# Optimization experiments

Hardware: AMD Instinct MI355X
Metric: run time of the kernel (lower is better)

## Reference

```python
import jax, jax.numpy as jnp
import numpy as np

TOP_K = 2


def setup_inputs() -> dict:
    key = jax.random.key(0)
    k1, k2, k3, k4, k5 = jax.random.split(key, 5)
    B, S, H, I, E = 2, 2048, 1024, 1408, 8
    scale = 0.02
    return {
        "hidden_states": jax.random.normal(k1, (B, S, H), dtype=jnp.float32),
        "router_w": jax.random.normal(k2, (E, H), dtype=jnp.float32) * scale,
        "w_gate": jax.random.normal(k3, (E, I, H), dtype=jnp.float32) * scale,
        "w_up": jax.random.normal(k4, (E, I, H), dtype=jnp.float32) * scale,
        "w_down": jax.random.normal(k5, (E, H, I), dtype=jnp.float32) * scale,
    }


def reference(hidden_states, router_w, w_gate, w_up, w_down):
    B, S, H = hidden_states.shape
    E = router_w.shape[0]
    x = hidden_states.reshape(-1, H)  # [T, H]

    # Router: softmax over experts, take top-k, renormalize.
    probs = jax.nn.softmax(x @ router_w.T, axis=-1)          # [T, E]
    topk_w, topk_idx = jax.lax.top_k(probs, TOP_K)            # [T, k]
    topk_w = topk_w / (jnp.sum(topk_w, axis=-1, keepdims=True) + 1e-20)

    # Dense combine weights: zero for non-selected experts -> identical math
    # to the masked gather/scatter loop in the original module.
    combine = jnp.sum(
        topk_w[..., None] * jax.nn.one_hot(topk_idx, E, dtype=topk_w.dtype),
        axis=1,
    )  # [T, E]

    out = jnp.zeros_like(x)
    for e in range(E):  # small fixed expert count; unrolled under jit
        g = x @ w_gate[e].T                                   # [T, I]
        u = x @ w_up[e].T                                     # [T, I]
        ye = (jax.nn.silu(g) * u) @ w_down[e].T               # [T, H]
        out = out + combine[:, e:e + 1] * ye
    return out.reshape(B, S, H)
```

## Files before the change

kernel.cpp:

```cpp
#include <hip/hip_runtime.h>
#include <hip/hip_bf16.h>

#define T_TOK 4096
#define H_DIM 1024
#define I_DIM 1408
#define E_NUM 8
#define P_CAP 8192
#define GRID_Y 71

typedef __bf16 bf16;
typedef __bf16 bf16x4 __attribute__((ext_vector_type(4)));
typedef __bf16 bf16x8 __attribute__((ext_vector_type(8)));
typedef float  f32x4  __attribute__((ext_vector_type(4)));

__device__ __forceinline__ void load_lds16(const void* g, void* l) {
  __builtin_amdgcn_global_load_lds((const __attribute__((address_space(1))) void*)g,
                                   (__attribute__((address_space(3))) void*)l, 16, 0, 0);
}

__global__ __launch_bounds__(256) void cast_all(const float* __restrict__ x,
                                                const float* __restrict__ wg,
                                                const float* __restrict__ wu,
                                                const float* __restrict__ wd,
                                                bf16* __restrict__ xb, bf16* __restrict__ wgb,
                                                bf16* __restrict__ wub, bf16* __restrict__ wdb) {
  int b = blockIdx.x;
  const float* s; bf16* d; int base;
  if (b < 4096)       { s = x;  d = xb;  base = b; }
  else if (b < 15360) { s = wg; d = wgb; base = b - 4096; }
  else if (b < 26624) { s = wu; d = wub; base = b - 15360; }
  else                { s = wd; d = wdb; base = b - 26624; }
  size_t i = ((size_t)base * 256 + threadIdx.x) * 4;
  float4 v = *(const float4*)(s + i);
  bf16x4 o;
  o.x = (bf16)v.x; o.y = (bf16)v.y; o.z = (bf16)v.z; o.w = (bf16)v.w;
  *(bf16x4*)(d + i) = o;
}

__global__ __launch_bounds__(256) void router_kernel(const float* __restrict__ x,
                                                     const float* __restrict__ rw,
                                                     int* __restrict__ tidx,
                                                     float* __restrict__ tw) {
  int t = blockIdx.x * 4 + (threadIdx.x >> 6);
  int lane = threadIdx.x & 63;
  const float* xr = x + (size_t)t * H_DIM;
  float acc[E_NUM];
#pragma unroll
  for (int e = 0; e < E_NUM; ++e) acc[e] = 0.f;
  for (int c = lane; c < H_DIM; c += 64) {
    float xv = xr[c];
#pragma unroll
    for (int e = 0; e < E_NUM; ++e) acc[e] += xv * rw[e * H_DIM + c];
  }
#pragma unroll
  for (int e = 0; e < E_NUM; ++e)
    for (int s = 32; s > 0; s >>= 1) acc[e] += __shfl_down(acc[e], s, 64);
  if (lane == 0) {
    int a = 0;
#pragma unroll
    for (int e = 1; e < E_NUM; ++e) if (acc[e] > acc[a]) a = e;
    int b = (a == 0) ? 1 : 0;
#pragma unroll
    for (int e = 0; e < E_NUM; ++e) if (e != a && acc[e] > acc[b]) b = e;
    float pb = expf(acc[b] - acc[a]);
    float inv = 1.f / (1.f + pb);
    tidx[t * 2] = a; tidx[t * 2 + 1] = b;
    tw[t * 2] = inv; tw[t * 2 + 1] = pb * inv;
  }
}

__global__ __launch_bounds__(256) void bucket_kernel(const int* __restrict__ tidx,
                                                     const float* __restrict__ tw,
                                                     int* __restrict__ pair_tok,
                                                     float* __restrict__ pair_w,
                                                     int* __restrict__ counts,
                                                     int* __restrict__ offsets,
                                                     int* __restrict__ blk2e,
                                                     int* __restrict__ blk2m) {
  __shared__ int sc[E_NUM], so[E_NUM], scur[E_NUM];
  int tid = threadIdx.x;
  if (tid < E_NUM) sc[tid] = 0;
  __syncthreads();
  for (int p = tid; p < T_TOK * 2; p += 256) atomicAdd(&sc[tidx[p]], 1);
  __syncthreads();
  if (tid == 0) {
    int run = 0, nb = 0;
    for (int e = 0; e < E_NUM; ++e) {
      so[e] = run; run += sc[e];
      for (int m = 0; m * 128 < sc[e]; ++m) { blk2e[nb] = e; blk2m[nb] = m; ++nb; }
    }
    for (; nb < GRID_Y; ++nb) { blk2e[nb] = -1; blk2m[nb] = 0; }
  }
  __syncthreads();
  if (tid < E_NUM) scur[tid] = so[tid];
  __syncthreads();
  for (int t = tid; t < T_TOK; t += 256) {
#pragma unroll
    for (int k = 0; k < 2; ++k) {
      int e = tidx[t * 2 + k];
      int pos = atomicAdd(&scur[e], 1);
      pair_tok[pos] = t;
      pair_w[pos] = tw[t * 2 + k];
    }
  }
  if (tid < E_NUM) { counts[tid] = sc[tid]; offsets[tid] = so[tid]; }
}

__global__ __launch_bounds__(256, 2)
void gemm1_kernel(const bf16* __restrict__ xb, const bf16* __restrict__ wgb,
                  const bf16* __restrict__ wub, const int* __restrict__ pair_tok,
                  const int* __restrict__ counts, const int* __restrict__ offsets,
                  const int* __restrict__ blk2e, const int* __restrict__ blk2m,
                  bf16* __restrict__ mid) {
  const int e = blk2e[blockIdx.y];
  if (e < 0) return;
  const int cnt = counts[e];
  const int m0 = blk2m[blockIdx.y] << 7;
  const int off = offsets[e];
  const int n0 = blockIdx.x << 7;

  __shared__ bf16 As[128 * 64];
  __shared__ bf16 Bgs[128 * 64];
  __shared__ bf16 Bus[128 * 64];

  const int tid = threadIdx.x;
  const int wave = tid >> 6;
  const int lane = tid & 63;
  const int wm = (wave >> 1) << 6;
  const int wn = (wave & 1) << 6;

  const bf16* wg_e = wgb + (size_t)e * (I_DIM * H_DIM);
  const bf16* wu_e = wub + (size_t)e * (I_DIM * H_DIM);

  int arow[4], acs[4], atok[4];
#pragma unroll
  for (int j = 0; j < 4; ++j) {
    int seg = ((wave << 2) + j) * 64 + lane;
    int row = seg >> 3;
    arow[j] = row;
    acs[j]  = ((seg & 7) ^ (row & 7)) << 3;
    int gr = m0 + row;
    int cr = gr < cnt ? gr : cnt - 1;
    atok[j] = pair_tok[off + cr];
  }

  f32x4 accg[4][4], accu[4][4];
#pragma unroll
  for (int i = 0; i < 4; ++i)
#pragma unroll
    for (int j = 0; j < 4; ++j) {
      accg[i][j] = (f32x4){0.f, 0.f, 0.f, 0.f};
      accu[i][j] = (f32x4){0.f, 0.f, 0.f, 0.f};
    }

  const int lr = lane & 15;
  const int sw = lr & 7;
  const int qd = lane >> 4;

  for (int k0 = 0; k0 < H_DIM; k0 += 64) {
#pragma unroll
    for (int j = 0; j < 4; ++j) {
      int base = ((wave << 2) + j) << 9;
      load_lds16(xb + (size_t)atok[j] * H_DIM + k0 + acs[j], As + base);
      load_lds16(wg_e + (size_t)(n0 + arow[j]) * H_DIM + k0 + acs[j], Bgs + base);
      load_lds16(wu_e + (size_t)(n0 + arow[j]) * H_DIM + k0 + acs[j], Bus + base);
    }
    __syncthreads();
#pragma unroll
    for (int ks = 0; ks < 2; ++ks) {
      const int kc = (((ks << 2) + qd) ^ sw) << 3;
      bf16x8 a[4], bg[4], bu[4];
#pragma unroll
      for (int i = 0; i < 4; ++i)
        a[i] = *(const bf16x8*)(As + (wm + (i << 4) + lr) * 64 + kc);
#pragma unroll
      for (int j = 0; j < 4; ++j) {
        bg[j] = *(const bf16x8*)(Bgs + (wn + (j << 4) + lr) * 64 + kc);
        bu[j] = *(const bf16x8*)(Bus + (wn + (j << 4) + lr) * 64 + kc);
      }
#pragma unroll
      for (int i = 0; i < 4; ++i)
#pragma unroll
        for (int j = 0; j < 4; ++j) {
          accg[i][j] = __builtin_amdgcn_mfma_f32_16x16x32_bf16(a[i], bg[j], accg[i][j], 0, 0, 0);
          accu[i][j] = __builtin_amdgcn_mfma_f32_16x16x32_bf16(a[i], bu[j], accu[i][j], 0, 0, 0);
        }
    }
    __syncthreads();
  }

#pragma unroll
  for (int i = 0; i < 4; ++i) {
#pragma unroll
    for (int r = 0; r < 4; ++r) {
      int row = wm + (i << 4) + (qd << 2) + r;
      int gr = m0 + row;
      if (gr < cnt) {
        bf16* mrow = mid + (size_t)(off + gr) * I_DIM + n0 + wn;
#pragma unroll
        for (int j = 0; j < 4; ++j) {
          float g = accg[i][j][r], u = accu[i][j][r];
          float s = g / (1.f + __expf(-g));
          mrow[(j << 4) + lr] = (bf16)(s * u);
        }
      }
    }
  }
}

__global__ __launch_bounds__(256, 2)
void gemm2_kernel(const bf16* __restrict__ mid, const bf16* __restrict__ wdb,
                  const int* __restrict__ pair_tok, const float* __restrict__ pair_w,
                  const int* __restrict__ counts, const int* __restrict__ offsets,
                  const int* __restrict__ blk2e, const int* __restrict__ blk2m,
                  float* __restrict__ out) {
  const int e = blk2e[blockIdx.y];
  if (e < 0) return;
  const int cnt = counts[e];
  const int m0 = blk2m[blockIdx.y] << 7;
  const int off = offsets[e];
  const int n0 = blockIdx.x << 7;

  __shared__ bf16 As[128 * 64];
  __shared__ bf16 Bs[128 * 64];

  const int tid = threadIdx.x;
  const int wave = tid >> 6;
  const int lane = tid & 63;
  const int wm = (wave >> 1) << 6;
  const int wn = (wave & 1) << 6;

  const bf16* wd_e = wdb + (size_t)e * (H_DIM * I_DIM);

  int arow[4], acs[4];
  size_t apos[4];
#pragma unroll
  for (int j = 0; j < 4; ++j) {
    int seg = ((wave << 2) + j) * 64 + lane;
    int row = seg >> 3;
    arow[j] = row;
    acs[j]  = ((seg & 7) ^ (row & 7)) << 3;
    int gr = m0 + row;
    int cr = gr < cnt ? gr : cnt - 1;
    apos[j] = (size_t)(off + cr) * I_DIM + acs[j];
  }

  f32x4 acc[4][4];
#pragma unroll
  for (int i = 0; i < 4; ++i)
#pragma unroll
    for (int j = 0; j < 4; ++j) acc[i][j] = (f32x4){0.f, 0.f, 0.f, 0.f};

  const int lr = lane & 15;
  const int sw = lr & 7;
  const int qd = lane >> 4;

  for (int k0 = 0; k0 < I_DIM; k0 += 64) {
#pragma unroll
    for (int j = 0; j < 4; ++j) {
      int base = ((wave << 2) + j) << 9;
      load_lds16(mid + apos[j] + k0, As + base);
      load_lds16(wd_e + (size_t)(n0 + arow[j]) * I_DIM + k0 + acs[j], Bs + base);
    }
    __syncthreads();
#pragma unroll
    for (int ks = 0; ks < 2; ++ks) {
      const int kc = (((ks << 2) + qd) ^ sw) << 3;
      bf16x8 a[4], b[4];
#pragma unroll
      for (int i = 0; i < 4; ++i)
        a[i] = *(const bf16x8*)(As + (wm + (i << 4) + lr) * 64 + kc);
#pragma unroll
      for (int j = 0; j < 4; ++j)
        b[j] = *(const bf16x8*)(Bs + (wn + (j << 4) + lr) * 64 + kc);
#pragma unroll
      for (int i = 0; i < 4; ++i)
#pragma unroll
        for (int j = 0; j < 4; ++j)
          acc[i][j] = __builtin_amdgcn_mfma_f32_16x16x32_bf16(a[i], b[j], acc[i][j], 0, 0, 0);
    }
    __syncthreads();
  }

#pragma unroll
  for (int i = 0; i < 4; ++i) {
#pragma unroll
    for (int r = 0; r < 4; ++r) {
      int row = wm + (i << 4) + (qd << 2) + r;
      int gr = m0 + row;
      if (gr < cnt) {
        int t = pair_tok[off + gr];
        float w = pair_w[off + gr];
        float* orow = out + (size_t)t * H_DIM + n0 + wn;
#pragma unroll
        for (int j = 0; j < 4; ++j)
          atomicAdd(orow + (j << 4) + lr, w * acc[i][j][r]);
      }
    }
  }
}

extern "C" void kernel_launch(void* const* d_in, const int* in_sizes, int n_in,
                              void* d_out, int out_size, void* d_ws, size_t ws_size,
                              hipStream_t stream) {
  const float* x  = (const float*)d_in[0];
  const float* rw = (const float*)d_in[1];
  const float* wg = (const float*)d_in[2];
  const float* wu = (const float*)d_in[3];
  const float* wd = (const float*)d_in[4];
  float* out = (float*)d_out;

  char* ws = (char*)d_ws;
  bf16*  xb      = (bf16*)(ws);
  bf16*  wgb     = (bf16*)(ws + 8388608);
  bf16*  wub     = (bf16*)(ws + 31457280);
  bf16*  wdb     = (bf16*)(ws + 54525952);
  bf16*  mid     = (bf16*)(ws + 77594624);
  int*   tidx    = (int*)(ws + 100663296);
  float* tw      = (float*)(ws + 100696064);
  int*   ptok    = (int*)(ws + 100728832);
  float* pw      = (float*)(ws + 100761600);
  int*   counts  = (int*)(ws + 100794368);
  int*   offsets = (int*)(ws + 100794400);
  int*   blk2e   = (int*)(ws + 100794432);
  int*   blk2m   = (int*)(ws + 100794752);

  hipMemsetAsync(d_out, 0, (size_t)T_TOK * H_DIM * sizeof(float), stream);
  cast_all<<<37888, 256, 0, stream>>>(x, wg, wu, wd, xb, wgb, wub, wdb);
  router_kernel<<<1024, 256, 0, stream>>>(x, rw, tidx, tw);
  bucket_kernel<<<1, 256, 0, stream>>>(tidx, tw, ptok, pw, counts, offsets, blk2e, blk2m);
  gemm1_kernel<<<dim3(11, GRID_Y), 256, 0, stream>>>(xb, wgb, wub, ptok, counts, offsets, blk2e, blk2m, mid);
  gemm2_kernel<<<dim3(8, GRID_Y), 256, 0, stream>>>(mid, wdb, ptok, pw, counts, offsets, blk2e, blk2m, out);
}
```

Before: 345.8 us.

## Replace atomic scatter with per-pair output buffer and gather combine kernel

gemm2 now writes each expert-pair result row to a dense fp32 buffer (reusing the wgb region, which is dead by then), and a new combine kernel gathers the two rows per token and applies the routing weights. This removes the output memset and the fp32 atomicAdd scatter. Block scheduling changes to a flattened, XCD-interleaved schedule table so blocks sharing an expert's weights land on the same chiplet. Bucketing uses wave ballots, and the router uses float4 loads. The cost is an extra 32MB write and read of intermediates plus one more kernel launch.

```diff
diff --git a/kernel.cpp b/kernel.cpp
--- a/kernel.cpp
+++ b/kernel.cpp
@@ -6,7 +6,8 @@
 #define I_DIM 1408
 #define E_NUM 8
 #define P_CAP 8192
-#define GRID_Y 71
+#define G1_GRID 1136
+#define G2_GRID 568
 
 typedef __bf16 bf16;
 typedef __bf16 bf16x4 __attribute__((ext_vector_type(4)));
@@ -43,14 +44,18 @@
                                                      float* __restrict__ tw) {
   int t = blockIdx.x * 4 + (threadIdx.x >> 6);
   int lane = threadIdx.x & 63;
-  const float* xr = x + (size_t)t * H_DIM;
+  const float4* xr  = (const float4*)(x + (size_t)t * H_DIM);
+  const float4* rw4 = (const float4*)rw;
   float acc[E_NUM];
 #pragma unroll
   for (int e = 0; e < E_NUM; ++e) acc[e] = 0.f;
-  for (int c = lane; c < H_DIM; c += 64) {
-    float xv = xr[c];
-#pragma unroll
-    for (int e = 0; e < E_NUM; ++e) acc[e] += xv * rw[e * H_DIM + c];
+  for (int c = lane; c < H_DIM / 4; c += 64) {
+    float4 xv = xr[c];
+#pragma unroll
+    for (int e = 0; e < E_NUM; ++e) {
+      float4 rv = rw4[e * (H_DIM / 4) + c];
+      acc[e] += xv.x * rv.x + xv.y * rv.y + xv.z * rv.z + xv.w * rv.w;
+    }
   }
 #pragma unroll
   for (int e = 0; e < E_NUM; ++e)
@@ -70,54 +75,90 @@
 }
 
 __global__ __launch_bounds__(256) void bucket_kernel(const int* __restrict__ tidx,
-                                                     const float* __restrict__ tw,
                                                      int* __restrict__ pair_tok,
-                                                     float* __restrict__ pair_w,
+                                                     int* __restrict__ inv,
                                                      int* __restrict__ counts,
                                                      int* __restrict__ offsets,
-                                                     int* __restrict__ blk2e,
-                                                     int* __restrict__ blk2m) {
+                                                     int* __restrict__ sched1,
+                                                     int* __restrict__ sched2) {
   __shared__ int sc[E_NUM], so[E_NUM], scur[E_NUM];
-  int tid = threadIdx.x;
+  int tid = threadIdx.x, lane = tid & 63, wv = tid >> 6;
   if (tid < E_NUM) sc[tid] = 0;
+  for (int i = tid; i < G1_GRID; i += 256) sched1[i] = -1;
+  for (int i = tid; i < G2_GRID; i += 256) sched2[i] = -1;
   __syncthreads();
-  for (int p = tid; p < T_TOK * 2; p += 256) atomicAdd(&sc[tidx[p]], 1);
+  int local[E_NUM];
+#pragma unroll
+  for (int e = 0; e < E_NUM; ++e) local[e] = 0;
+  for (int base = wv * 64; base < P_CAP; base += 256) {
+    int e = tidx[base + lane];
+#pragma unroll
+    for (int x = 0; x < E_NUM; ++x)
+      local[x] += __popcll(__ballot(e == x));
+  }
+  if (lane == 0) {
+#pragma unroll
+    for (int x = 0; x < E_NUM; ++x) atomicAdd(&sc[x], local[x]);
+  }
   __syncthreads();
   if (tid == 0) {
-    int run = 0, nb = 0;
-    for (int e = 0; e < E_NUM; ++e) {
-      so[e] = run; run += sc[e];
-      for (int m = 0; m * 128 < sc[e]; ++m) { blk2e[nb] = e; blk2m[nb] = m; ++nb; }
-    }
-    for (; nb < GRID_Y; ++nb) { blk2e[nb] = -1; blk2m[nb] = 0; }
+    int run = 0;
+    for (int e = 0; e < E_NUM; ++e) { so[e] = run; run += sc[e]; }
+    int q1[8] = {0,0,0,0,0,0,0,0};
+    for (int c = 0; c < 88; ++c) {
+      int e = c / 11, n0 = c % 11, k = c % 8;
+      for (int m = 0; m * 128 < sc[e]; ++m) {
+        sched1[q1[k] * 8 + k] = (e << 16) | (m << 8) | n0;
+        ++q1[k];
+      }
+    }
+    int q2[8] = {0,0,0,0,0,0,0,0};
+    for (int c = 0; c < 64; ++c) {
+      int e = c >> 3, n0 = c & 7, k = n0;
+      for (int m = 0; m * 128 < sc[e]; ++m) {
+        sched2[q2[k] * 8 + k] = (e << 16) | (m << 8) | n0;
+        ++q2[k];
+      }
+    }
   }
   __syncthreads();
-  if (tid < E_NUM) scur[tid] = so[tid];
+  if (tid < E_NUM) { scur[tid] = so[tid]; counts[tid] = sc[tid]; offsets[tid] = so[tid]; }
   __syncthreads();
-  for (int t = tid; t < T_TOK; t += 256) {
-#pragma unroll
-    for (int k = 0; k < 2; ++k) {
-      int e = tidx[t * 2 + k];
-      int pos = atomicAdd(&scur[e], 1);
-      pair_tok[pos] = t;
-      pair_w[pos] = tw[t * 2 + k];
-    }
-  }
-  if (tid < E_NUM) { counts[tid] = sc[tid]; offsets[tid] = so[tid]; }
+  for (int base = wv * 64; base < P_CAP; base += 256) {
+    int p = base + lane;
+    int e = tidx[p];
+#pragma unroll
+    for (int x = 0; x < E_NUM; ++x) {
+      bool mine = (e == x);
+      unsigned long long m = __ballot(mine);
+      if (m == 0) continue;
+      int leader = __ffsll((long long)m) - 1;
+      int n = __popcll(m);
+      int bpos = 0;
+      if (lane == leader) bpos = atomicAdd(&scur[x], n);
+      bpos = __shfl(bpos, leader, 64);
+      if (mine) {
+        int rank = __popcll(m & ((1ull << lane) - 1ull));
+        int pos = bpos + rank;
+        pair_tok[pos] = p >> 1;
+        inv[p] = pos;
+      }
+    }
+  }
 }
 
 __global__ __launch_bounds__(256, 2)
 void gemm1_kernel(const bf16* __restrict__ xb, const bf16* __restrict__ wgb,
                   const bf16* __restrict__ wub, const int* __restrict__ pair_tok,
                   const int* __restrict__ counts, const int* __restrict__ offsets,
-                  const int* __restrict__ blk2e, const int* __restrict__ blk2m,
-                  bf16* __restrict__ mid) {
-  const int e = blk2e[blockIdx.y];
-  if (e < 0) return;
+                  const int* __restrict__ sched1, bf16* __restrict__ mid) {
+  const int sv = sched1[blockIdx.x];
+  if (sv < 0) return;
+  const int e  = sv >> 16;
+  const int m0 = ((sv >> 8) & 0xff) << 7;
+  const int n0 = (sv & 0xff) << 7;
   const int cnt = counts[e];
-  const int m0 = blk2m[blockIdx.y] << 7;
   const int off = offsets[e];
-  const int n0 = blockIdx.x << 7;
 
   __shared__ bf16 As[128 * 64];
   __shared__ bf16 Bgs[128 * 64];
@@ -210,16 +251,15 @@
 
 __global__ __launch_bounds__(256, 2)
 void gemm2_kernel(const bf16* __restrict__ mid, const bf16* __restrict__ wdb,
-                  const int* __restrict__ pair_tok, const float* __restrict__ pair_w,
                   const int* __restrict__ counts, const int* __restrict__ offsets,
-                  const int* __restrict__ blk2e, const int* __restrict__ blk2m,
-                  float* __restrict__ out) {
-  const int e = blk2e[blockIdx.y];
-  if (e < 0) return;
+                  const int* __restrict__ sched2, float* __restrict__ ybuf) {
+  const int sv = sched2[blockIdx.x];
+  if (sv < 0) return;
+  const int e  = sv >> 16;
+  const int m0 = ((sv >> 8) & 0xff) << 7;
+  const int n0 = (sv & 0xff) << 7;
   const int cnt = counts[e];
-  const int m0 = blk2m[blockIdx.y] << 7;
   const int off = offsets[e];
-  const int n0 = blockIdx.x << 7;
 
   __shared__ bf16 As[128 * 64];
   __shared__ bf16 Bs[128 * 64];
@@ -289,15 +329,31 @@
       int row = wm + (i << 4) + (qd << 2) + r;
       int gr = m0 + row;
       if (gr < cnt) {
-        int t = pair_tok[off + gr];
-        float w = pair_w[off + gr];
-        float* orow = out + (size_t)t * H_DIM + n0 + wn;
+        float* yrow = ybuf + (size_t)(off + gr) * H_DIM + n0 + wn;
 #pragma unroll
         for (int j = 0; j < 4; ++j)
-          atomicAdd(orow + (j << 4) + lr, w * acc[i][j][r]);
-      }
-    }
-  }
+          yrow[(j << 4) + lr] = acc[i][j][r];
+      }
+    }
+  }
+}
+
+__global__ __launch_bounds__(256) void combine_kernel(const float* __restrict__ ybuf,
+                                                      const int* __restrict__ inv,
+                                                      const float* __restrict__ tw,
+                                                      float* __restrict__ out) {
+  int t = blockIdx.x;
+  int p0 = inv[2 * t], p1 = inv[2 * t + 1];
+  float w0 = tw[2 * t], w1 = tw[2 * t + 1];
+  int h = threadIdx.x * 4;
+  float4 a = *(const float4*)(ybuf + (size_t)p0 * H_DIM + h);
+  float4 b = *(const float4*)(ybuf + (size_t)p1 * H_DIM + h);
+  float4 o;
+  o.x = w0 * a.x + w1 * b.x;
+  o.y = w0 * a.y + w1 * b.y;
+  o.z = w0 * a.z + w1 * b.z;
+  o.w = w0 * a.w + w1 * b.w;
+  *(float4*)(out + (size_t)t * H_DIM + h) = o;
 }
 
 extern "C" void kernel_launch(void* const* d_in, const int* in_sizes, int n_in,
@@ -316,19 +372,20 @@
   bf16*  wub     = (bf16*)(ws + 31457280);
   bf16*  wdb     = (bf16*)(ws + 54525952);
   bf16*  mid     = (bf16*)(ws + 77594624);
+  float* ybuf    = (float*)(ws + 8388608);
   int*   tidx    = (int*)(ws + 100663296);
   float* tw      = (float*)(ws + 100696064);
   int*   ptok    = (int*)(ws + 100728832);
-  float* pw      = (float*)(ws + 100761600);
+  int*   inv     = (int*)(ws + 100761600);
   int*   counts  = (int*)(ws + 100794368);
   int*   offsets = (int*)(ws + 100794400);
-  int*   blk2e   = (int*)(ws + 100794432);
-  int*   blk2m   = (int*)(ws + 100794752);
-
-  hipMemsetAsync(d_out, 0, (size_t)T_TOK * H_DIM * sizeof(float), stream);
+  int*   sched1  = (int*)(ws + 100794432);
+  int*   sched2  = (int*)(ws + 100798976);
+
   cast_all<<<37888, 256, 0, stream>>>(x, wg, wu, wd, xb, wgb, wub, wdb);
   router_kernel<<<1024, 256, 0, stream>>>(x, rw, tidx, tw);
-  bucket_kernel<<<1, 256, 0, stream>>>(tidx, tw, ptok, pw, counts, offsets, blk2e, blk2m);
-  gemm1_kernel<<<dim3(11, GRID_Y), 256, 0, stream>>>(xb, wgb, wub, ptok, counts, offsets, blk2e, blk2m, mid);
-  gemm2_kernel<<<dim3(8, GRID_Y), 256, 0, stream>>>(mid, wdb, ptok, pw, counts, offsets, blk2e, blk2m, out);
-}
+  bucket_kernel<<<1, 256, 0, stream>>>(tidx, ptok, inv, counts, offsets, sched1, sched2);
+  gemm1_kernel<<<G1_GRID, 256, 0, stream>>>(xb, wgb, wub, ptok, counts, offsets, sched1, mid);
+  gemm2_kernel<<<G2_GRID, 256, 0, stream>>>(mid, wdb, counts, offsets, sched2, ybuf);
+  combine_kernel<<<T_TOK, 256, 0, stream>>>(ybuf, inv, tw, out);
+}
```

After: 453.0 us. +31.0%, slower.
